# Kernel tuning notes

Hardware: AMD Instinct MI355X
Metric: run time of the kernel (lower is better)

The kernel has to match this reference:

```python
import jax, jax.numpy as jnp
import numpy as np

BATCH, N_GRAPHS, N_NODES, UNITS = 512, 3, 4096, 256

def setup_inputs() -> dict:
    key = jax.random.key(0)
    ks = jax.random.split(key, 11)
    return {
        "inputs": jax.random.normal(ks[0], (BATCH, N_NODES), jnp.float32),
        "state": jax.random.normal(ks[1], (BATCH, UNITS), jnp.float32),
        "adj": jax.random.uniform(ks[2], (N_GRAPHS, N_NODES, N_NODES), jnp.float32),
        "wa": jax.random.uniform(ks[3], (N_GRAPHS,), jnp.float32),
        "w_gcn": jax.random.normal(ks[4], (N_NODES, UNITS), jnp.float32) * (1.0 / np.sqrt(N_NODES)),
        "wz": jax.random.normal(ks[5], (UNITS, UNITS), jnp.float32) * 0.05,
        "uz": jax.random.normal(ks[6], (UNITS, UNITS), jnp.float32) * 0.05,
        "bz": jax.random.normal(ks[7], (UNITS,), jnp.float32) * 0.05,
        "wh": jax.random.normal(ks[8], (UNITS, UNITS), jnp.float32) * 0.05,
        "uh": jax.random.normal(ks[9], (UNITS, UNITS), jnp.float32) * 0.05,
        "bh": jax.random.normal(ks[10], (UNITS,), jnp.float32) * 0.05,
    }

def reference(inputs, state, adj, wa, w_gcn, wz, uz, bz, wh, uh, bh):
    # Weighted sum of the n_graphs adjacency matrices: [g],[g,n,n] -> [n,n]
    adj_mix = jnp.einsum('g,gnm->nm', wa, adj)
    # Graph conv: (inputs @ adj_mix) @ w_gcn, then ReLU -> [batch, units]
    x = jax.nn.relu(jnp.matmul(jnp.matmul(inputs, adj_mix), w_gcn))
    # GRU-style gating
    z = jax.nn.sigmoid(x @ wz + state @ uz + bz)
    h_tilde = jnp.tanh(x @ wh + state @ uh + bh)
    out = (1.0 - z) * state + z * h_tilde
    return out
```

## Files before the change

kernel.cpp:

```cpp
#include <hip/hip_runtime.h>
#include <stdint.h>

typedef _Float16 f16;
typedef __attribute__((ext_vector_type(8))) _Float16 f16x8;
typedef __attribute__((ext_vector_type(4))) float f32x4;

#define NN 4096
#define UN 256

__device__ __forceinline__ f16x8 ld_f16x8(const f16* p){ return *(const f16x8*)p; }
__device__ __forceinline__ f32x4 zero4(){ f32x4 z = {0.f,0.f,0.f,0.f}; return z; }


__global__ __launch_bounds__(256) void k0_prep(
    const float* __restrict__ wg, const float* __restrict__ wz,
    const float* __restrict__ uz, const float* __restrict__ wh,
    const float* __restrict__ uh,
    f16* __restrict__ wgB,
    f16* __restrict__ czB_h, f16* __restrict__ czB_l,
    f16* __restrict__ chB_h, f16* __restrict__ chB_l)
{
  __shared__ float lsA[32*256];
  __shared__ float lsB[32*256];
  const int t = threadIdx.x;
  const int b = blockIdx.x;
  if (b < 128){
    const int kcg = b;
    #pragma unroll 8
    for (int i = 0; i < 32; i++)
      lsA[i*256 + t] = wg[(size_t)(kcg*32 + i) * UN + t];
    __syncthreads();
    #pragma unroll
    for (int i = 0; i < 4; i++){
      int o = i*256 + t;
      int l = o & 63;
      int n = ((o >> 6) << 4) + (l & 15);
      int kl = (l >> 4) * 8;
      f16 v8[8];
      #pragma unroll
      for (int j = 0; j < 8; j++) v8[j] = (f16)lsA[(kl + j)*256 + n];
      *(uint4*)(wgB + ((size_t)kcg*1024 + o)*8) = *(const uint4*)v8;
    }
  } else {
    const int kcg = b - 128;
    #pragma unroll 8
    for (int i = 0; i < 32; i++){
      int kg = kcg*32 + i;
      lsA[i*256 + t] = (kg < 256) ? wz[(size_t)kg * UN + t]
                                  : uz[(size_t)(kg - 256) * UN + t];
      lsB[i*256 + t] = (kg < 256) ? wh[(size_t)kg * UN + t]
                                  : uh[(size_t)(kg - 256) * UN + t];
    }
    __syncthreads();
    #pragma unroll
    for (int i = 0; i < 4; i++){
      int o = i*256 + t;
      int l = o & 63;
      int n = ((o >> 6) << 4) + (l & 15);
      int kl = (l >> 4) * 8;
      f16 zh[8], zl[8], hh[8], hl[8];
      #pragma unroll
      for (int j = 0; j < 8; j++){
        float vz = lsA[(kl + j)*256 + n];
        float vh = lsB[(kl + j)*256 + n];
        f16 a = (f16)vz; zh[j] = a; zl[j] = (f16)(vz - (float)a);
        f16 c = (f16)vh; hh[j] = c; hl[j] = (f16)(vh - (float)c);
      }
      size_t off = ((size_t)kcg*1024 + o)*8;
      *(uint4*)(czB_h + off) = *(const uint4*)zh;
      *(uint4*)(czB_l + off) = *(const uint4*)zl;
      *(uint4*)(chB_h + off) = *(const uint4*)hh;
      *(uint4*)(chB_l + off) = *(const uint4*)hl;
    }
  }
}

__global__ __launch_bounds__(256) void k1_w2(
    const float* __restrict__ adj, const float* __restrict__ wa,
    const f16* __restrict__ wgB, float* __restrict__ W2p)
{
  const int t = threadIdx.x, lane = t & 63, wv = t >> 6;
  const int qm = lane & 15, quad = lane >> 4;
  const int mbase = blockIdx.x * 64 + wv * 16;
  const int kbase = blockIdx.y * 512;
  const float wa0 = wa[0], wa1 = wa[1], wa2 = wa[2];
  const size_t gs = (size_t)NN * NN;
  const float* pa = adj + (size_t)(mbase + qm) * NN + kbase + quad * 8;

  f32x4 acc[16];
  #pragma unroll
  for (int i = 0; i < 16; i++) acc[i] = zero4();

  f32x4 g[6];
  #pragma unroll
  for (int r = 0; r < 2; r++)
    #pragma unroll
    for (int gi = 0; gi < 3; gi++)
      g[gi*2 + r] = *(const f32x4*)(pa + (size_t)gi*gs + r*4);

  for (int step = 0; step < 16; step++){
    const int kc = step * 32;
    const int kcg = (kbase + kc) >> 5;
    const f16* pb = wgB + ((size_t)kcg*1024 + lane)*8;

    f16x8 bf[8];
    #pragma unroll
    for (int i = 0; i < 8; i++) bf[i] = ld_f16x8(pb + i*512);

    f16x8 ah, al;
    #pragma unroll
    for (int j = 0; j < 4; j++){
      float v0 = wa0*g[0][j] + wa1*g[2][j] + wa2*g[4][j];
      float v1 = wa0*g[1][j] + wa1*g[3][j] + wa2*g[5][j];
      f16 h0 = (f16)v0, h1 = (f16)v1;
      ah[j] = h0;   al[j] = (f16)(v0 - (float)h0);
      ah[4+j] = h1; al[4+j] = (f16)(v1 - (float)h1);
    }

    f32x4 gn[6];
    if (step < 15){
      const float* pan = pa + kc + 32;
      #pragma unroll
      for (int r = 0; r < 2; r++)
        #pragma unroll
        for (int gi = 0; gi < 3; gi++)
          gn[gi*2 + r] = *(const f32x4*)(pan + (size_t)gi*gs + r*4);
    }

    f16x8 bg[8];
    #pragma unroll
    for (int i = 0; i < 8; i++) bg[i] = ld_f16x8(pb + (8+i)*512);

    #pragma unroll
    for (int tn = 0; tn < 8; tn++){
      acc[tn] = __builtin_amdgcn_mfma_f32_16x16x32_f16(ah, bf[tn], acc[tn], 0, 0, 0);
      acc[tn] = __builtin_amdgcn_mfma_f32_16x16x32_f16(al, bf[tn], acc[tn], 0, 0, 0);
    }
    #pragma unroll
    for (int tn = 0; tn < 8; tn++){
      acc[8+tn] = __builtin_amdgcn_mfma_f32_16x16x32_f16(ah, bg[tn], acc[8+tn], 0, 0, 0);
      acc[8+tn] = __builtin_amdgcn_mfma_f32_16x16x32_f16(al, bg[tn], acc[8+tn], 0, 0, 0);
    }

    #pragma unroll
    for (int i = 0; i < 6; i++) g[i] = gn[i];
  }

  float* wout = W2p + (size_t)blockIdx.y * ((size_t)NN * UN);
  #pragma unroll
  for (int tn = 0; tn < 16; tn++)
    #pragma unroll
    for (int r = 0; r < 4; r++)
      wout[(size_t)(mbase + quad*4 + r)*UN + tn*16 + qm] = acc[tn][r];
}

__global__ __launch_bounds__(256) void k_cvt(
    const float* __restrict__ W2p, f16* __restrict__ W2B)
{
  __shared__ float ls[32*256];
  const int t = threadIdx.x;
  const int kcg = blockIdx.x;
  const int r0 = t >> 6;
  const int c0 = (t & 63) * 4;
  #pragma unroll
  for (int i = 0; i < 8; i++){
    int r = i*4 + r0;
    const float* src = W2p + (size_t)(kcg*32 + r) * UN + c0;
    f32x4 s = zero4();
    #pragma unroll
    for (int p = 0; p < 8; p++)
      s = s + *(const f32x4*)(src + (size_t)p * ((size_t)NN*UN));
    *(f32x4*)(ls + r*256 + c0) = s;
  }
  __syncthreads();
  #pragma unroll
  for (int i = 0; i < 4; i++){
    int o = i*256 + t;
    int l = o & 63;
    int n = ((o >> 6) << 4) + (l & 15);
    int kl = (l >> 4) * 8;
    f16 v8[8];
    #pragma unroll
    for (int j = 0; j < 8; j++) v8[j] = (f16)ls[(kl + j)*256 + n];
    *(uint4*)(W2B + ((size_t)kcg*1024 + o)*8) = *(const uint4*)v8;
  }
}

__global__ __launch_bounds__(256) void k2_x(
    const float* __restrict__ inputs, const f16* __restrict__ W2B,
    float* __restrict__ xgp)
{
  const int t = threadIdx.x, lane = t & 63, wv = t >> 6;
  const int qm = lane & 15, quad = lane >> 4;
  const int m0 = blockIdx.x * 16;
  const int kbase = blockIdx.y * 512;
  const float* pa = inputs + (size_t)(m0 + qm) * NN + kbase + quad * 8;

  f32x4 acc[4] = { zero4(), zero4(), zero4(), zero4() };

  #pragma unroll 4
  for (int kc = 0; kc < 512; kc += 32){
    f32x4 a0 = *(const f32x4*)(pa + kc);
    f32x4 a1 = *(const f32x4*)(pa + kc + 4);
    const int kcg = (kbase + kc) >> 5;
    const f16* pb = W2B + (((size_t)kcg*16 + wv*4)*64 + lane)*8;
    f16x8 bfr[4];
    #pragma unroll
    for (int tn = 0; tn < 4; tn++) bfr[tn] = ld_f16x8(pb + tn*512);
    f16x8 ah, al;
    #pragma unroll
    for (int j = 0; j < 4; j++){
      f16 h0 = (f16)a0[j], h1 = (f16)a1[j];
      ah[j] = h0;   al[j] = (f16)(a0[j] - (float)h0);
      ah[4+j] = h1; al[4+j] = (f16)(a1[j] - (float)h1);
    }
    #pragma unroll
    for (int tn = 0; tn < 4; tn++){
      acc[tn] = __builtin_amdgcn_mfma_f32_16x16x32_f16(ah, bfr[tn], acc[tn], 0, 0, 0);
      acc[tn] = __builtin_amdgcn_mfma_f32_16x16x32_f16(al, bfr[tn], acc[tn], 0, 0, 0);
    }
  }
  float* xo = xgp + (size_t)blockIdx.y * ((size_t)512 * UN);
  #pragma unroll
  for (int tn = 0; tn < 4; tn++)
    #pragma unroll
    for (int r = 0; r < 4; r++)
      xo[(size_t)(m0 + quad*4 + r)*UN + (wv*4 + tn)*16 + qm] = acc[tn][r];
}

__global__ __launch_bounds__(256) void k_tail(
    const float* __restrict__ xgp, const float* __restrict__ state,
    const f16* __restrict__ czB_h, const f16* __restrict__ czB_l,
    const f16* __restrict__ chB_h, const f16* __restrict__ chB_l,
    const float* __restrict__ bz, const float* __restrict__ bh,
    float* __restrict__ out)
{
  __shared__ f16 xah[16][520];
  __shared__ f16 xal[16][520];
  const int t = threadIdx.x;
  const int m0 = blockIdx.x * 16;

  {
    const int r = t >> 4, cb = (t & 15) * 16;
    #pragma unroll
    for (int cc = 0; cc < 16; cc += 4){
      const int c = cb + cc;
      const float* src = xgp + (size_t)(m0 + r) * UN + c;
      f32x4 s = zero4();
      #pragma unroll
      for (int p = 0; p < 8; p++)
        s = s + *(const f32x4*)(src + (size_t)p * (512*UN));
      f16 h4[4], l4[4];
      #pragma unroll
      for (int j = 0; j < 4; j++){
        float v = fmaxf(s[j], 0.f);
        f16 hh = (f16)v; h4[j] = hh; l4[j] = (f16)(v - (float)hh);
      }
      *(uint2*)&xah[r][c] = *(const uint2*)h4;
      *(uint2*)&xal[r][c] = *(const uint2*)l4;
      f32x4 st = *(const f32x4*)(state + (size_t)(m0 + r) * UN + c);
      #pragma unroll
      for (int j = 0; j < 4; j++){
        f16 hh = (f16)st[j]; h4[j] = hh; l4[j] = (f16)(st[j] - (float)hh);
      }
      *(uint2*)&xah[r][256 + c] = *(const uint2*)h4;
      *(uint2*)&xal[r][256 + c] = *(const uint2*)l4;
    }
  }
  __syncthreads();

  const int lane = t & 63, wv = t >> 6;
  const int qm = lane & 15, quad = lane >> 4;
  f32x4 az[4] = { zero4(), zero4(), zero4(), zero4() };
  f32x4 ag[4] = { zero4(), zero4(), zero4(), zero4() };

  for (int kb = 0; kb < 512; kb += 32){
    f16x8 ah = *(const f16x8*)&xah[qm][kb + quad*8];
    f16x8 al = *(const f16x8*)&xal[qm][kb + quad*8];
    const int kcg = kb >> 5;
    const size_t base = (((size_t)kcg*16 + wv*4)*64 + lane)*8;
    #pragma unroll
    for (int tn = 0; tn < 4; tn++){
      f16x8 bzh = ld_f16x8(czB_h + base + tn*512);
      f16x8 bzl = ld_f16x8(czB_l + base + tn*512);
      f16x8 bhh = ld_f16x8(chB_h + base + tn*512);
      f16x8 bhl = ld_f16x8(chB_l + base + tn*512);
      az[tn] = __builtin_amdgcn_mfma_f32_16x16x32_f16(ah, bzh, az[tn], 0, 0, 0);
      az[tn] = __builtin_amdgcn_mfma_f32_16x16x32_f16(al, bzh, az[tn], 0, 0, 0);
      az[tn] = __builtin_amdgcn_mfma_f32_16x16x32_f16(ah, bzl, az[tn], 0, 0, 0);
      ag[tn] = __builtin_amdgcn_mfma_f32_16x16x32_f16(ah, bhh, ag[tn], 0, 0, 0);
      ag[tn] = __builtin_amdgcn_mfma_f32_16x16x32_f16(al, bhh, ag[tn], 0, 0, 0);
      ag[tn] = __builtin_amdgcn_mfma_f32_16x16x32_f16(ah, bhl, ag[tn], 0, 0, 0);
    }
  }

  #pragma unroll
  for (int tn = 0; tn < 4; tn++){
    const int col = (wv*4 + tn)*16 + qm;
    const float bzv = bz[col], bhv = bh[col];
    #pragma unroll
    for (int r = 0; r < 4; r++){
      const int row = m0 + quad*4 + r;
      const float s = state[(size_t)row*UN + col];
      float z = 1.f / (1.f + __expf(-(az[tn][r] + bzv)));
      float ex = __expf(2.f * (ag[tn][r] + bhv));
      float hh = 1.f - 2.f / (ex + 1.f);
      out[(size_t)row*UN + col] = (1.f - z) * s + z * hh;
    }
  }
}

extern "C" void kernel_launch(void* const* d_in, const int* in_sizes, int n_in,
                              void* d_out, int out_size, void* d_ws, size_t ws_size,
                              hipStream_t stream)
{
  const float* inputs = (const float*)d_in[0];
  const float* state  = (const float*)d_in[1];
  const float* adj    = (const float*)d_in[2];
  const float* wa     = (const float*)d_in[3];
  const float* wg     = (const float*)d_in[4];
  const float* wz     = (const float*)d_in[5];
  const float* uz     = (const float*)d_in[6];
  const float* bz     = (const float*)d_in[7];
  const float* wh     = (const float*)d_in[8];
  const float* uh     = (const float*)d_in[9];
  const float* bh     = (const float*)d_in[10];
  float* out = (float*)d_out;

  char* ws = (char*)d_ws;
  float* W2p   = (float*)(ws);
  float* xgp   = (float*)(ws + (32u<<20));
  f16* wgB     = (f16*)(ws + (36u<<20));
  f16* W2B     = (f16*)(ws + (38u<<20));
  f16* czB_h   = (f16*)(ws + (40u<<20));
  f16* czB_l   = (f16*)(ws + (40u<<20) + (256u<<10));
  f16* chB_h   = (f16*)(ws + (40u<<20) + (512u<<10));
  f16* chB_l   = (f16*)(ws + (40u<<20) + (768u<<10));

  k0_prep<<<144, 256, 0, stream>>>(wg, wz, uz, wh, uh,
                                   wgB, czB_h, czB_l, chB_h, chB_l);
  k1_w2<<<dim3(64, 8), 256, 0, stream>>>(adj, wa, wgB, W2p);
  k_cvt<<<128, 256, 0, stream>>>(W2p, W2B);
  k2_x<<<dim3(32, 8), 256, 0, stream>>>(inputs, W2B, xgp);
  k_tail<<<32, 256, 0, stream>>>(xgp, state, czB_h, czB_l, chB_h, chB_l,
                                 bz, bh, out);
}
```

Before: 377.9 us.

## Split GRU tail kernel over column quarters and K-split across waves

The tail kernel now launches a 32x4 grid, so each block handles 64 output columns instead of all 256. Inside a block the four waves split the K dimension and reduce their partial results through shared memory. The epilogue is vectorized with f32x4 loads and stores. This is meant to fill more of the GPU than 32 blocks can, at the cost of redundant xgp reduction and f16 conversion per column quarter plus an extra shared-memory reduction and barrier.

```diff
diff --git a/kernel.cpp b/kernel.cpp
--- a/kernel.cpp
+++ b/kernel.cpp
@@ -228,17 +228,20 @@
       xo[(size_t)(m0 + quad*4 + r)*UN + (wv*4 + tn)*16 + qm] = acc[tn][r];
 }
 
-__global__ __launch_bounds__(256) void k_tail(
+__global__ __launch_bounds__(256) void k3_out(
     const float* __restrict__ xgp, const float* __restrict__ state,
     const f16* __restrict__ czB_h, const f16* __restrict__ czB_l,
     const f16* __restrict__ chB_h, const f16* __restrict__ chB_l,
     const float* __restrict__ bz, const float* __restrict__ bh,
     float* __restrict__ out)
 {
-  __shared__ f16 xah[16][520];
-  __shared__ f16 xal[16][520];
+  __shared__ __align__(16) f16 xah[16][520];
+  __shared__ __align__(16) f16 xal[16][520];
+  __shared__ __align__(16) float rz[4][16][68];
+  __shared__ __align__(16) float rh[4][16][68];
   const int t = threadIdx.x;
   const int m0 = blockIdx.x * 16;
+  const int nq = blockIdx.y;
 
   {
     const int r = t >> 4, cb = (t & 15) * 16;
@@ -274,11 +277,13 @@
   f32x4 az[4] = { zero4(), zero4(), zero4(), zero4() };
   f32x4 ag[4] = { zero4(), zero4(), zero4(), zero4() };
 
-  for (int kb = 0; kb < 512; kb += 32){
+  #pragma unroll
+  for (int j = 0; j < 4; j++){
+    const int kb = wv*128 + j*32;
     f16x8 ah = *(const f16x8*)&xah[qm][kb + quad*8];
     f16x8 al = *(const f16x8*)&xal[qm][kb + quad*8];
     const int kcg = kb >> 5;
-    const size_t base = (((size_t)kcg*16 + wv*4)*64 + lane)*8;
+    const size_t base = (((size_t)kcg*16 + nq*4)*64 + lane)*8;
     #pragma unroll
     for (int tn = 0; tn < 4; tn++){
       f16x8 bzh = ld_f16x8(czB_h + base + tn*512);
@@ -295,18 +300,35 @@
   }
 
   #pragma unroll
-  for (int tn = 0; tn < 4; tn++){
-    const int col = (wv*4 + tn)*16 + qm;
-    const float bzv = bz[col], bhv = bh[col];
+  for (int tn = 0; tn < 4; tn++)
     #pragma unroll
     for (int r = 0; r < 4; r++){
-      const int row = m0 + quad*4 + r;
-      const float s = state[(size_t)row*UN + col];
-      float z = 1.f / (1.f + __expf(-(az[tn][r] + bzv)));
-      float ex = __expf(2.f * (ag[tn][r] + bhv));
+      rz[wv][quad*4 + r][tn*16 + qm] = az[tn][r];
+      rh[wv][quad*4 + r][tn*16 + qm] = ag[tn][r];
+    }
+  __syncthreads();
+
+  {
+    const int row = t >> 4, c0 = (t & 15) * 4;
+    f32x4 z4 = zero4(), h4 = zero4();
+    #pragma unroll
+    for (int w = 0; w < 4; w++){
+      z4 = z4 + *(const f32x4*)&rz[w][row][c0];
+      h4 = h4 + *(const f32x4*)&rh[w][row][c0];
+    }
+    const int gcol = nq*64 + c0;
+    f32x4 s4  = *(const f32x4*)(state + (size_t)(m0 + row)*UN + gcol);
+    f32x4 bz4 = *(const f32x4*)(bz + gcol);
+    f32x4 bh4 = *(const f32x4*)(bh + gcol);
+    f32x4 o4;
+    #pragma unroll
+    for (int j = 0; j < 4; j++){
+      float z = 1.f / (1.f + __expf(-(z4[j] + bz4[j])));
+      float ex = __expf(2.f * (h4[j] + bh4[j]));
       float hh = 1.f - 2.f / (ex + 1.f);
-      out[(size_t)row*UN + col] = (1.f - z) * s + z * hh;
-    }
+      o4[j] = (1.f - z) * s4[j] + z * hh;
+    }
+    *(f32x4*)(out + (size_t)(m0 + row)*UN + gcol) = o4;
   }
 }
 
@@ -342,6 +364,6 @@
   k1_w2<<<dim3(64, 8), 256, 0, stream>>>(adj, wa, wgB, W2p);
   k_cvt<<<128, 256, 0, stream>>>(W2p, W2B);
   k2_x<<<dim3(32, 8), 256, 0, stream>>>(inputs, W2B, xgp);
-  k_tail<<<32, 256, 0, stream>>>(xgp, state, czB_h, czB_l, chB_h, chB_l,
-                                 bz, bh, out);
-}
+  k3_out<<<dim3(32, 4), 256, 0, stream>>>(xgp, state, czB_h, czB_l,
+                                          chB_h, chB_l, bz, bh, out);
+}
```

Result: faster. 350.5 us (-7.3%).
